# Performance work log

Hardware: AMD Instinct MI355X
Metric: run time of the kernel (lower is better)

The kernel has to match this reference:

```python
import jax, jax.numpy as jnp
import numpy as np


def setup_inputs() -> dict:
    key = jax.random.key(0)
    kx, ky = jax.random.split(key)
    N, M, D = 16384, 16384, 512
    x = jax.random.normal(kx, (N, D), dtype=jnp.float32)
    y = jax.random.normal(ky, (M, D), dtype=jnp.float32)
    return {"x": x, "y": y, "device": 0}


def reference(x, y, device):
    # torch.cdist(x, y, p=2): pairwise Euclidean distances [N, M]
    # matching torch's large-matrix cdist path), clamped for numerical safety.
    x_sq = jnp.sum(x * x, axis=1, keepdims=True)          # [N, 1]
    y_sq = jnp.sum(y * y, axis=1)                          # [M]
    sq_dists = x_sq + y_sq[None, :] - 2.0 * (x @ y.T)      # [N, M]
    dists = jnp.sqrt(jnp.maximum(sq_dists, 0.0))
    # min over centers (dim=1), then argmax over candidates (dim=0)
    min_dists = jnp.min(dists, axis=1)                     # [N]
    max_id = jnp.argmax(min_dists)
    max_val = min_dists[max_id]
    return max_val, max_id
```

## Files before the change

kernel.cpp:

```cpp
#include <hip/hip_runtime.h>
#include <hip/hip_fp8.h>
#include <math.h>

#define N_ROWS 16384
#define M_ROWS 16384
#define DIM    512
#define JS     8
#define KCAND  256
#define DELTA  0.40f

typedef __attribute__((ext_vector_type(8))) int   int8v;
typedef __attribute__((ext_vector_type(4))) int   int4v;
typedef __attribute__((ext_vector_type(4))) float floatx4;

__global__ __launch_bounds__(256) void convert_kernel(const float* __restrict__ x, const float* __restrict__ y,
                                                      unsigned char* __restrict__ xh8, unsigned char* __restrict__ yh8,
                                                      float* __restrict__ x_sq, float* __restrict__ y_sq,
                                                      unsigned int* __restrict__ gmax_bits,
                                                      unsigned int* __restrict__ cnt, int* __restrict__ cand) {
    if (blockIdx.x == 0) {
        if (threadIdx.x < KCAND) cand[threadIdx.x] = 0;
        if (threadIdx.x == 0) { *gmax_bits = 0u; *cnt = 0u; }
    }
    int wave = threadIdx.x >> 6, lane = threadIdx.x & 63;
    int row = blockIdx.x * 4 + wave;
    const float* src; unsigned char* dst8; float* dsq; int r;
    if (row < N_ROWS) { r = row;          src = x; dst8 = xh8; dsq = x_sq; }
    else              { r = row - N_ROWS; src = y; dst8 = yh8; dsq = y_sq; }
    const float4* s4 = (const float4*)(src + (size_t)r * DIM);
    float4 a = s4[lane * 2];
    float4 b = s4[lane * 2 + 1];
    float v[8] = {a.x, a.y, a.z, a.w, b.x, b.y, b.z, b.w};
    union { unsigned char b[8]; uint2 u2; } pk;
    float s = 0.f;
    #pragma unroll
    for (int i = 0; i < 8; ++i) {
        s += v[i] * v[i];
        __hip_fp8_e4m3 q(v[i]);
        pk.b[i] = (unsigned char)q.__x;
    }
    *(uint2*)(dst8 + (size_t)r * DIM + lane * 8) = pk.u2;
    #pragma unroll
    for (int off = 32; off > 0; off >>= 1) s += __shfl_down(s, off, 64);
    if (lane == 0) dsq[r] = s;
}

__global__ __launch_bounds__(256, 2) void pass1_kernel(const unsigned char* __restrict__ xh8,
                                                       const unsigned char* __restrict__ yh8,
                                                       const float* __restrict__ y_sq,
                                                       float* __restrict__ part) {
    __shared__ __align__(16) unsigned char Bs[4][16384];
    __shared__ __align__(16) float ysq_s[M_ROWS / JS];
    __shared__ float red[2][128];

    const int t = threadIdx.x;
    const int w = t >> 6, lane = t & 63;
    const int col = lane & 15, q = lane >> 4;
    const int h = w >> 1, c = w & 1;

    const int bid = blockIdx.x;
    const int wg = (bid & 7) * 128 + (bid >> 3);
    const int js = wg >> 7;
    const int i0 = (wg & 127) * 128;
    const int jbase = js * (M_ROWS / JS);

    {
        const float4* ys4 = (const float4*)(y_sq + jbase);
        float4 v0 = ys4[t * 2];
        float4 v1 = ys4[t * 2 + 1];
        *(float4*)&ysq_s[t * 8]     = v0;
        *(float4*)&ysq_s[t * 8 + 4] = v1;
    }

    {
        const unsigned char* gs = xh8 + (size_t)i0 * DIM;
        unsigned char* ls = (unsigned char*)Bs;
        #pragma unroll
        for (int it = 0; it < 16; ++it) {
            int s  = it * 256 + t;
            int r  = s >> 5;
            int u  = s & 31;
            int kq = u >> 3;
            int cl = (u & 7) ^ (r & 7);
            __builtin_amdgcn_global_load_lds(
                (const __attribute__((address_space(1))) void*)(gs + r * 512 + kq * 128 + cl * 16),
                (__attribute__((address_space(3))) void*)(ls + it * 4096 + w * 1024),
                16, 0, 0);
        }
    }
    __syncthreads();

    int8v afr[4][4];
    {
        const unsigned char* ab = (const unsigned char*)Bs;
        #pragma unroll
        for (int mt = 0; mt < 4; ++mt) {
            int rr = h * 64 + mt * 16 + col;
            #pragma unroll
            for (int kc = 0; kc < 4; ++kc) {
                int base = rr * 512 + kc * 128 + (((q << 1) ^ (rr & 7)) << 4);
                int4v a0 = *(const int4v*)(ab + base);
                int4v a1 = *(const int4v*)(ab + (base ^ 16));
                int8v f;
                f[0] = a0[0]; f[1] = a0[1]; f[2] = a0[2]; f[3] = a0[3];
                f[4] = a1[0]; f[5] = a1[1]; f[6] = a1[2]; f[7] = a1[3];
                afr[mt][kc] = f;
            }
        }
    }
    __syncthreads();

    int spo[4];
    {
        #pragma unroll
        for (int i = 0; i < 4; ++i) {
            int s  = w * 256 + i * 64 + lane;
            int g  = s >> 7, u = s & 127;
            int jl = (g << 4) + (u & 15);
            int p  = (u >> 4) ^ (u & 7);
            spo[i] = jl * DIM + p * 16;
        }
    }
    const unsigned char* tb = yh8 + (size_t)jbase * DIM;
    const int Klane = col * 16 + (((q << 1) ^ (col & 7)) << 8);

    float minv[16];
    #pragma unroll
    for (int i = 0; i < 16; ++i) minv[i] = __builtin_inff();

#define STAGE(BUF, TOFF)                                                                     \
    { _Pragma("unroll")                                                                      \
      for (int i_ = 0; i_ < 4; ++i_) {                                                       \
          __builtin_amdgcn_global_load_lds(                                                  \
              (const __attribute__((address_space(1))) void*)(tb + spo[i_] + (TOFF)),        \
              (__attribute__((address_space(3))) void*)(&Bs[BUF][w * 4096 + i_ * 1024]),     \
              16, 0, 0);                                                                     \
      } }

    STAGE(0, 0)
    STAGE(1, 128)

    for (int jt = 0; jt < 16; ++jt) {
        floatx4 acc[4][4];
        #pragma unroll
        for (int mt = 0; mt < 4; ++mt)
            #pragma unroll
            for (int nt = 0; nt < 4; ++nt) acc[mt][nt] = (floatx4){0.f, 0.f, 0.f, 0.f};
        #pragma unroll
        for (int kc = 0; kc < 4; ++kc) {
            const int jtp  = (jt + (kc >> 1)) & 15;
            const int toff = jtp * (128 * DIM) + (((kc + 2) & 3) << 7);
            STAGE((kc + 2) & 3, toff)
            asm volatile("s_waitcnt vmcnt(8)" ::: "memory");
            __builtin_amdgcn_s_barrier();
            asm volatile("" ::: "memory");
            #pragma unroll
            for (int nt = 0; nt < 4; ++nt) {
                const unsigned char* gb = &Bs[kc][(c * 4 + nt) * 2048];
                int4v lo = *(const int4v*)(gb + Klane);
                int4v hi = *(const int4v*)(gb + (Klane ^ 256));
                int8v b;
                b[0] = lo[0]; b[1] = lo[1]; b[2] = lo[2]; b[3] = lo[3];
                b[4] = hi[0]; b[5] = hi[1]; b[6] = hi[2]; b[7] = hi[3];
                __builtin_amdgcn_s_setprio(1);
                #pragma unroll
                for (int mt = 0; mt < 4; ++mt)
                    acc[mt][nt] = __builtin_amdgcn_mfma_scale_f32_16x16x128_f8f6f4(
                        afr[mt][kc], b, acc[mt][nt], 0, 0, 0, 127, 0, 127);
                __builtin_amdgcn_s_setprio(0);
            }
        }
        #pragma unroll
        for (int nt = 0; nt < 4; ++nt) {
            float qv = ysq_s[jt * 128 + c * 64 + nt * 16 + col];
            #pragma unroll
            for (int mt = 0; mt < 4; ++mt)
                #pragma unroll
                for (int r = 0; r < 4; ++r)
                    minv[mt * 4 + r] = fminf(minv[mt * 4 + r], qv - 2.f * acc[mt][nt][r]);
        }
    }
#undef STAGE

    #pragma unroll
    for (int i = 0; i < 16; ++i) {
        float v = minv[i];
        v = fminf(v, __shfl_xor(v, 1, 64));
        v = fminf(v, __shfl_xor(v, 2, 64));
        v = fminf(v, __shfl_xor(v, 4, 64));
        v = fminf(v, __shfl_xor(v, 8, 64));
        minv[i] = v;
    }
    if (col == 0) {
        #pragma unroll
        for (int mt = 0; mt < 4; ++mt)
            #pragma unroll
            for (int r = 0; r < 4; ++r)
                red[c][h * 64 + mt * 16 + q * 4 + r] = minv[mt * 4 + r];
    }
    __syncthreads();
    if (t < 128)
        part[(size_t)(i0 + t) * JS + js] = fminf(red[0][t], red[1][t]);
}

__global__ __launch_bounds__(1024) void maxred_kernel(const float* __restrict__ part,
                                                      const float* __restrict__ x_sq,
                                                      float* __restrict__ aval,
                                                      unsigned int* __restrict__ gmax_bits) {
    __shared__ float sm[1024];
    int t = threadIdx.x;
    int row = blockIdx.x * 1024 + t;
    float m = part[(size_t)row * JS];
    #pragma unroll
    for (int c = 1; c < JS; ++c) m = fminf(m, part[(size_t)row * JS + c]);
    float v = sqrtf(fmaxf(x_sq[row] + m, 0.f));
    aval[row] = v;
    sm[t] = v;
    __syncthreads();
    for (int s = 512; s > 0; s >>= 1) {
        if (t < s) sm[t] = fmaxf(sm[t], sm[t + s]);
        __syncthreads();
    }
    if (t == 0) atomicMax(gmax_bits, __float_as_uint(sm[0]));
}

__global__ __launch_bounds__(1024) void select_kernel(const float* __restrict__ aval,
                                                      const unsigned int* __restrict__ gmax_bits,
                                                      unsigned int* __restrict__ cnt,
                                                      int* __restrict__ cand) {
    int row = blockIdx.x * 1024 + threadIdx.x;
    float gmax = __uint_as_float(*gmax_bits);
    if (aval[row] >= gmax - DELTA) {
        unsigned s = atomicAdd(cnt, 1u);
        if (s < KCAND) cand[s] = row;
    }
}

#define TIr 64
#define LDA 68
#define LDB 132
__global__ __launch_bounds__(256) void rescore_kernel(const float* __restrict__ x, const float* __restrict__ y,
                                                      const float* __restrict__ y_sq,
                                                      const int* __restrict__ cand,
                                                      const unsigned int* __restrict__ cnt,
                                                      float* __restrict__ part2) {
    __shared__ __align__(16) float As[32 * LDA];
    __shared__ __align__(16) float Bs[32 * LDB];
    __shared__ float red[TIr][17];

    int t = threadIdx.x;
    int tx = t & 15, ty = t >> 4;
    int i0 = blockIdx.x * TIr;
    int j0 = blockIdx.y * 128;

    if ((unsigned)i0 >= *cnt) return;

    float acc[4][8];
    #pragma unroll
    for (int c = 0; c < 4; ++c)
        #pragma unroll
        for (int d = 0; d < 8; ++d) acc[c][d] = 0.f;

    int srow = t >> 3;
    int skq = (t & 7) * 4;
    int grow0 = cand[i0 + srow];
    int grow1 = cand[i0 + 32 + srow];

    for (int kc = 0; kc < DIM; kc += 32) {
        {
            float4 v = *(const float4*)(x + (size_t)grow0 * DIM + kc + skq);
            As[(skq + 0) * LDA + srow] = v.x;
            As[(skq + 1) * LDA + srow] = v.y;
            As[(skq + 2) * LDA + srow] = v.z;
            As[(skq + 3) * LDA + srow] = v.w;
            v = *(const float4*)(x + (size_t)grow1 * DIM + kc + skq);
            As[(skq + 0) * LDA + 32 + srow] = v.x;
            As[(skq + 1) * LDA + 32 + srow] = v.y;
            As[(skq + 2) * LDA + 32 + srow] = v.z;
            As[(skq + 3) * LDA + 32 + srow] = v.w;
        }
        #pragma unroll
        for (int it = 0; it < 4; ++it) {
            int row = it * 32 + srow;
            float4 v = *(const float4*)(y + (size_t)(j0 + row) * DIM + kc + skq);
            Bs[(skq + 0) * LDB + row] = v.x;
            Bs[(skq + 1) * LDB + row] = v.y;
            Bs[(skq + 2) * LDB + row] = v.z;
            Bs[(skq + 3) * LDB + row] = v.w;
        }
        __syncthreads();
        #pragma unroll 8
        for (int k = 0; k < 32; ++k) {
            float4 a  = *(const float4*)&As[k * LDA + ty * 4];
            float4 b0 = *(const float4*)&Bs[k * LDB + tx * 8];
            float4 b1 = *(const float4*)&Bs[k * LDB + tx * 8 + 4];
            float av[4] = {a.x, a.y, a.z, a.w};
            float bv[8] = {b0.x, b0.y, b0.z, b0.w, b1.x, b1.y, b1.z, b1.w};
            #pragma unroll
            for (int c = 0; c < 4; ++c)
                #pragma unroll
                for (int d = 0; d < 8; ++d)
                    acc[c][d] = fmaf(av[c], bv[d], acc[c][d]);
        }
        __syncthreads();
    }

    float4 q0 = *(const float4*)(y_sq + j0 + tx * 8);
    float4 q1 = *(const float4*)(y_sq + j0 + tx * 8 + 4);
    float qv[8] = {q0.x, q0.y, q0.z, q0.w, q1.x, q1.y, q1.z, q1.w};
    float mv[4] = {__builtin_inff(), __builtin_inff(), __builtin_inff(), __builtin_inff()};
    #pragma unroll
    for (int c = 0; c < 4; ++c)
        #pragma unroll
        for (int d = 0; d < 8; ++d)
            mv[c] = fminf(mv[c], qv[d] - 2.f * acc[c][d]);
    #pragma unroll
    for (int c = 0; c < 4; ++c) red[ty * 4 + c][tx] = mv[c];
    __syncthreads();
    if (t < TIr) {
        float m = red[t][0];
        #pragma unroll
        for (int xx = 1; xx < 16; ++xx) m = fminf(m, red[t][xx]);
        part2[(size_t)(i0 + t) * 128 + blockIdx.y] = m;
    }
}

__global__ __launch_bounds__(256) void final2_kernel(const float* __restrict__ part2,
                                                     const float* __restrict__ x_sq,
                                                     const int* __restrict__ cand,
                                                     const unsigned int* __restrict__ cnt,
                                                     float* __restrict__ out) {
    __shared__ float sv[256];
    __shared__ int si[256];
    int t = threadIdx.x;
    const float4* p4 = (const float4*)(part2 + (size_t)t * 128);
    float m = __builtin_inff();
    for (int c = 0; c < 32; ++c) {
        float4 v = p4[c];
        m = fminf(m, fminf(fminf(v.x, v.y), fminf(v.z, v.w)));
    }
    unsigned n = *cnt;
    if (n > KCAND) n = KCAND;
    int row = cand[t];
    float v = (t < (int)n) ? sqrtf(fmaxf(x_sq[row] + m, 0.f)) : -__builtin_inff();
    sv[t] = v; si[t] = row;
    __syncthreads();
    for (int s = 128; s > 0; s >>= 1) {
        if (t < s) {
            float v2 = sv[t + s]; int i2 = si[t + s];
            if (v2 > sv[t] || (v2 == sv[t] && i2 < si[t])) { sv[t] = v2; si[t] = i2; }
        }
        __syncthreads();
    }
    if (t == 0) { out[0] = sv[0]; out[1] = (float)si[0]; }
}

extern "C" void kernel_launch(void* const* d_in, const int* in_sizes, int n_in,
                              void* d_out, int out_size, void* d_ws, size_t ws_size,
                              hipStream_t stream) {
    const float* x = (const float*)d_in[0];
    const float* y = (const float*)d_in[1];
    float* out = (float*)d_out;

    char* w = (char*)d_ws;
    unsigned char* xh8 = (unsigned char*)w;
    unsigned char* yh8 = (unsigned char*)(w + (size_t)8388608);
    float* x_sq = (float*)(w + (size_t)16777216);
    float* y_sq = x_sq + N_ROWS;
    float* part = y_sq + M_ROWS;
    float* aval = part + (size_t)N_ROWS * JS;
    float* part2 = aval + N_ROWS;
    int* cand = (int*)(part2 + KCAND * 128);
    unsigned int* gmax_bits = (unsigned int*)(cand + KCAND);
    unsigned int* cnt = gmax_bits + 1;

    convert_kernel<<<(N_ROWS + M_ROWS) / 4, 256, 0, stream>>>(x, y, xh8, yh8, x_sq, y_sq, gmax_bits, cnt, cand);
    pass1_kernel<<<1024, 256, 0, stream>>>(xh8, yh8, y_sq, part);
    maxred_kernel<<<N_ROWS / 1024, 1024, 0, stream>>>(part, x_sq, aval, gmax_bits);
    select_kernel<<<N_ROWS / 1024, 1024, 0, stream>>>(aval, gmax_bits, cnt, cand);
    dim3 g2(KCAND / TIr, M_ROWS / 128);
    rescore_kernel<<<g2, 256, 0, stream>>>(x, y, y_sq, cand, cnt, part2);
    final2_kernel<<<1, 256, 0, stream>>>(part2, x_sq, cand, cnt, out);
}
```

Measured before the change: 269.8 us.

## Restructure LDS staging into two half-tile phases with fewer barriers

```diff
diff --git a/kernel.cpp b/kernel.cpp
--- a/kernel.cpp
+++ b/kernel.cpp
@@ -137,8 +137,28 @@
               16, 0, 0);                                                                     \
       } }
 
+#define COMPUTE(KC)                                                                          \
+    { _Pragma("unroll")                                                                      \
+      for (int nt = 0; nt < 4; ++nt) {                                                       \
+          const unsigned char* gb = &Bs[KC][(c * 4 + nt) * 2048];                            \
+          int4v lo = *(const int4v*)(gb + Klane);                                            \
+          int4v hi = *(const int4v*)(gb + (Klane ^ 256));                                    \
+          int8v b;                                                                           \
+          b[0] = lo[0]; b[1] = lo[1]; b[2] = lo[2]; b[3] = lo[3];                            \
+          b[4] = hi[0]; b[5] = hi[1]; b[6] = hi[2]; b[7] = hi[3];                            \
+          __builtin_amdgcn_s_setprio(1);                                                     \
+          _Pragma("unroll")                                                                  \
+          for (int mt = 0; mt < 4; ++mt)                                                     \
+              acc[mt][nt] = __builtin_amdgcn_mfma_scale_f32_16x16x128_f8f6f4(                \
+                  afr[mt][KC], b, acc[mt][nt], 0, 0, 0, 127, 0, 127);                        \
+          __builtin_amdgcn_s_setprio(0);                                                     \
+      } }
+
     STAGE(0, 0)
     STAGE(1, 128)
+    asm volatile("s_waitcnt vmcnt(0)" ::: "memory");
+    __builtin_amdgcn_s_barrier();
+    asm volatile("" ::: "memory");
 
     for (int jt = 0; jt < 16; ++jt) {
         floatx4 acc[4][4];
@@ -146,30 +166,29 @@
         for (int mt = 0; mt < 4; ++mt)
             #pragma unroll
             for (int nt = 0; nt < 4; ++nt) acc[mt][nt] = (floatx4){0.f, 0.f, 0.f, 0.f};
-        #pragma unroll
-        for (int kc = 0; kc < 4; ++kc) {
-            const int jtp  = (jt + (kc >> 1)) & 15;
-            const int toff = jtp * (128 * DIM) + (((kc + 2) & 3) << 7);
-            STAGE((kc + 2) & 3, toff)
-            asm volatile("s_waitcnt vmcnt(8)" ::: "memory");
-            __builtin_amdgcn_s_barrier();
-            asm volatile("" ::: "memory");
-            #pragma unroll
-            for (int nt = 0; nt < 4; ++nt) {
-                const unsigned char* gb = &Bs[kc][(c * 4 + nt) * 2048];
-                int4v lo = *(const int4v*)(gb + Klane);
-                int4v hi = *(const int4v*)(gb + (Klane ^ 256));
-                int8v b;
-                b[0] = lo[0]; b[1] = lo[1]; b[2] = lo[2]; b[3] = lo[3];
-                b[4] = hi[0]; b[5] = hi[1]; b[6] = hi[2]; b[7] = hi[3];
-                __builtin_amdgcn_s_setprio(1);
-                #pragma unroll
-                for (int mt = 0; mt < 4; ++mt)
-                    acc[mt][nt] = __builtin_amdgcn_mfma_scale_f32_16x16x128_f8f6f4(
-                        afr[mt][kc], b, acc[mt][nt], 0, 0, 0, 127, 0, 127);
-                __builtin_amdgcn_s_setprio(0);
-            }
-        }
+
+        {
+            const int ta = jt * (128 * DIM);
+            STAGE(2, ta + 256)
+            STAGE(3, ta + 384)
+        }
+        COMPUTE(0)
+        COMPUTE(1)
+        asm volatile("s_waitcnt vmcnt(0)" ::: "memory");
+        __builtin_amdgcn_s_barrier();
+        asm volatile("" ::: "memory");
+
+        {
+            const int tb2 = ((jt + 1) & 15) * (128 * DIM);
+            STAGE(0, tb2)
+            STAGE(1, tb2 + 128)
+        }
+        COMPUTE(2)
+        COMPUTE(3)
+        asm volatile("s_waitcnt vmcnt(0)" ::: "memory");
+        __builtin_amdgcn_s_barrier();
+        asm volatile("" ::: "memory");
+
         #pragma unroll
         for (int nt = 0; nt < 4; ++nt) {
             float qv = ysq_s[jt * 128 + c * 64 + nt * 16 + col];
@@ -181,6 +200,7 @@
         }
     }
 #undef STAGE
+#undef COMPUTE
 
     #pragma unroll
     for (int i = 0; i < 16; ++i) {
```

Measured after the change: 275.7 us. 1.02x slower.
